# Kernel tuning notes

Hardware: AMD Instinct MI355X
Metric: run time of the kernel (lower is better)

The kernel has to match this reference:

```python
import jax, jax.numpy as jnp
import numpy as np

N, E, IN, HID, HEADS, LAYERS, CLASSES = 50000, 800000, 256, 128, 4, 3, 2
DH = HID // HEADS
EPS = 1e-5


def _layernorm(h, g, b):
    mu = jnp.mean(h, axis=-1, keepdims=True)
    var = jnp.mean(jnp.square(h - mu), axis=-1, keepdims=True)
    return (h - mu) / jnp.sqrt(var + EPS) * g + b


def setup_inputs() -> dict:
    key = jax.random.key(0)
    ks = jax.random.split(key, 16)

    def w(k, shape, fan_in):
        return jax.random.normal(k, shape, dtype=jnp.float32) / np.sqrt(fan_in).astype(np.float32)

    inp = {}
    inp["x"] = jax.random.normal(ks[0], (N, IN), dtype=jnp.float32)
    inp["edge_index"] = jax.random.randint(ks[1], (2, E), 0, N, dtype=jnp.int32)
    inp["batch"] = jnp.zeros((N,), dtype=jnp.int32)  # single graph
    # feature extractor: Linear(IN,HID) -> ReLU -> Linear(HID,HID)
    inp["fe_w1"] = w(ks[2], (HID, IN), IN)
    inp["fe_b1"] = jnp.zeros((HID,), jnp.float32)
    inp["fe_w2"] = w(ks[3], (HID, HID), HID)
    inp["fe_b2"] = jnp.zeros((HID,), jnp.float32)
    inp["conv_w"] = w(ks[4], (LAYERS, HID, 2 * HID), 2 * HID)
    inp["conv_b"] = jnp.zeros((LAYERS, HID), jnp.float32)
    inp["ln_g"] = jnp.ones((LAYERS, HID), jnp.float32)
    inp["ln_b"] = jnp.zeros((LAYERS, HID), jnp.float32)
    # MultiheadAttention(HID, 4 heads): packed in_proj + out_proj
    inp["in_proj_w"] = w(ks[5], (3 * HID, HID), HID)
    inp["in_proj_b"] = jnp.zeros((3 * HID,), jnp.float32)
    inp["out_w"] = w(ks[6], (HID, HID), HID)
    inp["out_b"] = jnp.zeros((HID,), jnp.float32)
    # classifier: Linear(2*HID, HID) -> ReLU -> Linear(HID, CLASSES)
    inp["c_w1"] = w(ks[7], (HID, 2 * HID), 2 * HID)
    inp["c_b1"] = jnp.zeros((HID,), jnp.float32)
    inp["c_w2"] = w(ks[8], (CLASSES, HID), HID)
    inp["c_b2"] = jnp.zeros((CLASSES,), jnp.float32)
    return inp


def reference(x, edge_index, batch, fe_w1, fe_b1, fe_w2, fe_b2, conv_w, conv_b,
              ln_g, ln_b, in_proj_w, in_proj_b, out_w, out_b, c_w1, c_b1, c_w2, c_b2):
    # feature extractor (dropout inactive in eval mode)
    h = jax.nn.relu(x @ fe_w1.T + fe_b1) @ fe_w2.T + fe_b2  # [N, HID]
    row, col = edge_index[0], edge_index[1]
    for i in range(LAYERS):
        # scatter_add of source-node features onto destination nodes
        nbr = jax.ops.segment_sum(h[row], col, num_segments=N)  # [N, HID]
        hcat = jnp.concatenate([h, nbr], axis=-1)               # [N, 2*HID]
        h = _layernorm(hcat @ conv_w[i].T + conv_b[i], ln_g[i], ln_b[i])
        h = jax.nn.relu(h)
    # MultiheadAttention with h.unsqueeze(0) and batch_first=False:
    # seq_len = 1, batch = N -> softmax over a single key yields weight 1.
    qkv = h @ in_proj_w.T + in_proj_b                          # [N, 3*HID]
    q, k, v = jnp.split(qkv, 3, axis=-1)
    qh = q.reshape(N, HEADS, DH)
    kh = k.reshape(N, HEADS, DH)
    vh = v.reshape(N, HEADS, DH)
    scores = jnp.sum(qh * kh, axis=-1) / np.sqrt(DH).astype(np.float32)  # [N, H]
    wts = jax.nn.softmax(scores[..., None], axis=-1)           # [N, H, 1] == 1
    attn = wts * vh                                            # [N, H, DH]
    h_attn = attn.reshape(N, HID) @ out_w.T + out_b
    h = h + h_attn
    # global mean / max pool over (all-zero) batch ids
    counts = jax.ops.segment_sum(jnp.ones((N, 1), h.dtype), batch, num_segments=1)
    h_mean = jax.ops.segment_sum(h, batch, num_segments=1) / counts      # [1, HID]
    h_max = jax.ops.segment_max(h, batch, num_segments=1)                # [1, HID]
    g = jnp.concatenate([h_mean, h_max], axis=-1)                        # [1, 2*HID]
    return jax.nn.relu(g @ c_w1.T + c_b1) @ c_w2.T + c_b2                # [1, CLASSES]
```

## Files before the change

### kernel.cpp

```cpp
#include <hip/hip_runtime.h>

constexpr int HID = 128;
constexpr int NB  = 1024;
constexpr int NCH = 64;

typedef __attribute__((ext_vector_type(8))) short short8;
typedef __attribute__((ext_vector_type(8))) unsigned short us8;
typedef __attribute__((ext_vector_type(4))) float f32x4;

__device__ __forceinline__ unsigned short f2bf(float f) {
    union { float f; unsigned u; } v; v.f = f;
    unsigned r = v.u + 0x7fffu + ((v.u >> 16) & 1u);
    return (unsigned short)(r >> 16);
}
__device__ __forceinline__ float bf2f(unsigned short u) {
    union { unsigned u; float f; } v; v.u = ((unsigned)u) << 16;
    return v.f;
}

template<int K, bool CONCAT, bool RELU, bool LN, bool POOL>
__device__ __forceinline__
void mgemm_body(int bid, const unsigned short* __restrict__ A1b,
                const unsigned short* __restrict__ A2b,
                const unsigned short* __restrict__ Wb,
                const float* __restrict__ bias, const float* __restrict__ lng,
                const float* __restrict__ lnb, unsigned short* __restrict__ C,
                float* __restrict__ part, int nrows)
{
    constexpr int LDT = 40;
    __shared__ unsigned short lds[2 * 128 * LDT];
    unsigned short* As = lds;
    unsigned short* Ws = lds + 128 * LDT;
    const int tid = threadIdx.x;
    const int w = tid >> 6, l = tid & 63;
    const int lr = l & 15, lg = l >> 4;
    const int row0 = bid * 128;

    f32x4 acc[2][8] = {};
    const int sr = tid >> 1;
    const int sc = (tid & 1) * 16;
    int gr = row0 + sr; if (gr >= nrows) gr = nrows - 1;

    for (int k0 = 0; k0 < K; k0 += 32) {
        const unsigned short* bsrc;
        if (CONCAT) bsrc = ((k0 < 128) ? A1b : A2b) + (size_t)gr * 128 + (k0 & 127) + sc;
        else        bsrc = A1b + (size_t)gr * K + k0 + sc;
        us8 a0 = *(const us8*)(bsrc + 0);
        us8 a1 = *(const us8*)(bsrc + 8);
        *(us8*)&As[sr * LDT + sc + 0] = a0;
        *(us8*)&As[sr * LDT + sc + 8] = a1;

        const unsigned short* s = Wb + (size_t)sr * K + k0 + sc;
        us8 b0 = *(const us8*)(s + 0);
        us8 b1 = *(const us8*)(s + 8);
        *(us8*)&Ws[sr * LDT + sc + 0] = b0;
        *(us8*)&Ws[sr * LDT + sc + 8] = b1;
        __syncthreads();

        short8 afr[2];
#pragma unroll
        for (int rt = 0; rt < 2; rt++)
            afr[rt] = *(const short8*)&As[(w * 32 + rt * 16 + lr) * LDT + lg * 8];
#pragma unroll
        for (int ct = 0; ct < 8; ct++) {
            short8 bfr = *(const short8*)&Ws[(ct * 16 + lr) * LDT + lg * 8];
#pragma unroll
            for (int rt = 0; rt < 2; rt++)
                acc[rt][ct] = __builtin_amdgcn_mfma_f32_16x16x32_bf16(
                    afr[rt], bfr, acc[rt][ct], 0, 0, 0);
        }
        __syncthreads();
    }

    float bia[8], g8[8], be[8];
#pragma unroll
    for (int ct = 0; ct < 8; ct++) {
        bia[ct] = bias[ct * 16 + lr];
        if (LN) { g8[ct] = lng[ct * 16 + lr]; be[ct] = lnb[ct * 16 + lr]; }
    }
    float ps[8], pm[8];
    if (POOL) {
#pragma unroll
        for (int ct = 0; ct < 8; ct++) { ps[ct] = 0.f; pm[ct] = -3.402823466e+38f; }
    }
#pragma unroll
    for (int rt = 0; rt < 2; rt++) {
#pragma unroll
        for (int r_ = 0; r_ < 4; r_++) {
            int row = row0 + w * 32 + rt * 16 + lg * 4 + r_;
            float v[8];
#pragma unroll
            for (int ct = 0; ct < 8; ct++) v[ct] = acc[rt][ct][r_] + bia[ct];
            if (LN) {
                float s = 0.f;
#pragma unroll
                for (int ct = 0; ct < 8; ct++) s += v[ct];
#pragma unroll
                for (int m = 8; m >= 1; m >>= 1) s += __shfl_xor(s, m);
                float mean = s * (1.f / 128.f);
                float q = 0.f;
#pragma unroll
                for (int ct = 0; ct < 8; ct++) { v[ct] -= mean; q += v[ct] * v[ct]; }
#pragma unroll
                for (int m = 8; m >= 1; m >>= 1) q += __shfl_xor(q, m);
                float rstd = rsqrtf(q * (1.f / 128.f) + 1e-5f);
#pragma unroll
                for (int ct = 0; ct < 8; ct++) v[ct] = v[ct] * rstd * g8[ct] + be[ct];
            }
            if (RELU) {
#pragma unroll
                for (int ct = 0; ct < 8; ct++) v[ct] = fmaxf(v[ct], 0.f);
            }
            if (row < nrows) {
                if (POOL) {
#pragma unroll
                    for (int ct = 0; ct < 8; ct++) {
                        ps[ct] += v[ct];
                        pm[ct] = fmaxf(pm[ct], v[ct]);
                    }
                } else {
#pragma unroll
                    for (int ct = 0; ct < 8; ct++)
                        C[(size_t)row * 128 + ct * 16 + lr] = f2bf(v[ct]);
                }
            }
        }
    }
    if (POOL) {
        float* scr = (float*)lds;
        const int g = w * 4 + lg;
#pragma unroll
        for (int ct = 0; ct < 8; ct++) {
            int col = ct * 16 + lr;
            scr[g * 128 + col] = ps[ct];
            scr[2048 + g * 128 + col] = pm[ct];
        }
        __syncthreads();
        if (tid < 128) {
            float s = 0.f, m = -3.402823466e+38f;
#pragma unroll
            for (int gg = 0; gg < 16; gg++) {
                s += scr[gg * 128 + tid];
                m = fmaxf(m, scr[2048 + gg * 128 + tid]);
            }
            part[bid * 256 + tid] = s;
            part[bid * 256 + 128 + tid] = m;
        }
    }
}

template<int K, bool CONCAT, bool RELU, bool LN, bool POOL>
__global__ __launch_bounds__(256)
void mgemm(const unsigned short* __restrict__ A1b, const unsigned short* __restrict__ A2b,
           const unsigned short* __restrict__ Wb, const float* __restrict__ bias,
           const float* __restrict__ lng, const float* __restrict__ lnb,
           unsigned short* __restrict__ C, float* __restrict__ part, int nrows)
{
    mgemm_body<K,CONCAT,RELU,LN,POOL>(blockIdx.x, A1b, A2b, Wb, bias, lng, lnb,
                                      C, part, nrows);
}

__device__ __forceinline__ void cvt8_blk(const float* __restrict__ src,
                                         unsigned short* __restrict__ dst,
                                         int relb, int n)
{
    int i = (relb * 256 + threadIdx.x) * 8;
    if (i + 8 <= n) {
        float4 a = *(const float4*)(src + i);
        float4 b = *(const float4*)(src + i + 4);
        us8 o;
        o[0]=f2bf(a.x); o[1]=f2bf(a.y); o[2]=f2bf(a.z); o[3]=f2bf(a.w);
        o[4]=f2bf(b.x); o[5]=f2bf(b.y); o[6]=f2bf(b.z); o[7]=f2bf(b.w);
        *(us8*)(dst + i) = o;
    } else {
        for (int j = i; j < n; j++) dst[j] = f2bf(src[j]);
    }
}

__global__ __launch_bounds__(256)
void prep0(const float* __restrict__ x, unsigned short* __restrict__ xb, int nx,
           const float* __restrict__ fe_w1, unsigned short* __restrict__ w1b,
           const float* __restrict__ fe_w2, unsigned short* __restrict__ w2b,
           const float* __restrict__ conv_w, unsigned short* __restrict__ cwb,
           const float* __restrict__ out_w, const float* __restrict__ v_w,
           const float* __restrict__ out_b, const float* __restrict__ bv,
           unsigned short* __restrict__ Mb, float* __restrict__ bias2,
           const int* __restrict__ ecol, int* __restrict__ ccnt,
           int range, int ch_sz, int E)
{
    const int b = blockIdx.x;
    const int tid = threadIdx.x;
    if (b < NCH) {
        __shared__ int cnt[NB];
        for (int i = tid; i < NB; i += 256) cnt[i] = 0;
        __syncthreads();
        int e0 = b * ch_sz;
        int e1 = e0 + ch_sz; if (e1 > E) e1 = E;
        int e = e0 + tid;
        for (; e + 768 < e1; e += 1024) {
            int c0 = ecol[e], c1 = ecol[e+256], c2 = ecol[e+512], c3 = ecol[e+768];
            atomicAdd(&cnt[c0 / range], 1);
            atomicAdd(&cnt[c1 / range], 1);
            atomicAdd(&cnt[c2 / range], 1);
            atomicAdd(&cnt[c3 / range], 1);
        }
        for (; e < e1; e += 256)
            atomicAdd(&cnt[ecol[e] / range], 1);
        __syncthreads();
        for (int i = tid; i < NB; i += 256) ccnt[(size_t)i * NCH + b] = cnt[i];
        return;
    }
    int b2 = b - NCH;
    if (b2 < 64) {
        const int i = b2 * 2 + (tid >> 7);
        const int j = tid & 127;
        float s = 0.f;
        for (int k = 0; k < 128; k++)
            s = fmaf(out_w[i*128 + k], v_w[k*128 + j], s);
        Mb[i*128 + j] = f2bf(s + ((i == j) ? 1.f : 0.f));
        if (j == 0) {
            float bb = out_b[i];
            for (int k = 0; k < 128; k++)
                bb = fmaf(out_w[i*128 + k], bv[k], bb);
            bias2[i] = bb;
        }
        return;
    }
    b2 -= 64;
    if (b2 < 16) { cvt8_blk(fe_w1, w1b, b2, 128*256); return; }
    b2 -= 16;
    if (b2 < 8)  { cvt8_blk(fe_w2, w2b, b2, 128*128); return; }
    b2 -= 8;
    if (b2 < 48) { cvt8_blk(conv_w, cwb, b2, 3*128*256); return; }
    b2 -= 48;
    cvt8_blk(x, xb, b2, nx);
}

__global__ __launch_bounds__(256)
void p2scan(const int* __restrict__ ccnt, int* __restrict__ cbase,
            int* __restrict__ btot, int* __restrict__ bbase)
{
    __shared__ int wsum[4];
    const int t = threadIdx.x;
    int tot[4];
#pragma unroll
    for (int j = 0; j < 4; j++) {
        int b = t * 4 + j;
        const int4* p = (const int4*)(ccnt + (size_t)b * NCH);
        int s = 0;
#pragma unroll
        for (int q = 0; q < NCH / 4; q++) {
            int4 v = p[q];
            s += (v.x + v.y) + (v.z + v.w);
        }
        tot[j] = s;
    }
    int tsum = tot[0] + tot[1] + tot[2] + tot[3];
    int inc = tsum;
#pragma unroll
    for (int d2 = 1; d2 < 64; d2 <<= 1) {
        int u = __shfl_up(inc, d2);
        if ((t & 63) >= d2) inc += u;
    }
    if ((t & 63) == 63) wsum[t >> 6] = inc;
    __syncthreads();
    int woff = 0;
#pragma unroll
    for (int w = 0; w < 4; w++) if (w < (t >> 6)) woff += wsum[w];
    int ex = woff + inc - tsum;
#pragma unroll
    for (int j = 0; j < 4; j++) {
        int b = t * 4 + j;
        bbase[b] = ex;
        btot[b]  = tot[j];
        const int4* p = (const int4*)(ccnt + (size_t)b * NCH);
        int4* q4 = (int4*)(cbase + (size_t)b * NCH);
        int run = ex;
#pragma unroll
        for (int q = 0; q < NCH / 4; q++) {
            int4 v = p[q];
            int4 o;
            o.x = run; run += v.x;
            o.y = run; run += v.y;
            o.z = run; run += v.z;
            o.w = run; run += v.w;
            q4[q] = o;
        }
        ex += tot[j];
    }
}

__global__ __launch_bounds__(256)
void fe1_scat(const unsigned short* __restrict__ xb, const unsigned short* __restrict__ w1b,
              const float* __restrict__ fe_b1, unsigned short* __restrict__ outh,
              int nrows,
              const int* __restrict__ erow, const int* __restrict__ ecol,
              const int* __restrict__ cbase, unsigned* __restrict__ grouped,
              int range, int ch_sz, int E)
{
    const int b = blockIdx.x;
    const int tid = threadIdx.x;
    if (b < NCH) {
        const int chunk = b;
        __shared__ int cur[NB];
        for (int i = tid; i < NB; i += 256) cur[i] = cbase[(size_t)i * NCH + chunk];
        __syncthreads();
        int e0 = chunk * ch_sz;
        int e1 = e0 + ch_sz; if (e1 > E) e1 = E;
        int e = e0 + tid;
        for (; e + 768 < e1; e += 1024) {
            int c0 = ecol[e],     r0 = erow[e];
            int c1 = ecol[e+256], r1 = erow[e+256];
            int c2 = ecol[e+512], r2 = erow[e+512];
            int c3 = ecol[e+768], r3 = erow[e+768];
            int bk0 = c0 / range, bk1 = c1 / range, bk2 = c2 / range, bk3 = c3 / range;
            int p0 = atomicAdd(&cur[bk0], 1);
            int p1 = atomicAdd(&cur[bk1], 1);
            int p2 = atomicAdd(&cur[bk2], 1);
            int p3 = atomicAdd(&cur[bk3], 1);
            grouped[p0] = ((unsigned)r0 << 6) | (unsigned)(c0 - bk0 * range);
            grouped[p1] = ((unsigned)r1 << 6) | (unsigned)(c1 - bk1 * range);
            grouped[p2] = ((unsigned)r2 << 6) | (unsigned)(c2 - bk2 * range);
            grouped[p3] = ((unsigned)r3 << 6) | (unsigned)(c3 - bk3 * range);
        }
        for (; e < e1; e += 256) {
            int c = ecol[e], r = erow[e];
            int bk = c / range;
            int pos = atomicAdd(&cur[bk], 1);
            grouped[pos] = ((unsigned)r << 6) | (unsigned)(c - bk * range);
        }
        return;
    }
    mgemm_body<256,false,true,false,false>(
        b - NCH, xb, nullptr, w1b, fe_b1, nullptr, nullptr, outh, nullptr, nrows);
}

__global__ __launch_bounds__(256)
void fe2_csr2(const unsigned short* __restrict__ hin, const unsigned short* __restrict__ w2b,
              const float* __restrict__ fe_b2, unsigned short* __restrict__ outh,
              int nrows, int nbk,
              const int* __restrict__ bbase, const int* __restrict__ btot,
              const unsigned* __restrict__ grouped, int range, int N,
              int* __restrict__ offg, int* __restrict__ degg, int* __restrict__ csr)
{
    const int b = blockIdx.x;
    const int tid = threadIdx.x;
    if (b >= nbk) {
        mgemm_body<128,false,false,false,false>(
            b - nbk, hin, nullptr, w2b, fe_b2, nullptr, nullptr, outh, nullptr, nrows);
        return;
    }
    const int bk = b;
    __shared__ unsigned ent[2048];
    __shared__ int hist[64];
    __shared__ int cur2[64];
    const int base = bbase[bk];
    int cnt = btot[bk]; if (cnt > 2048) cnt = 2048;
    for (int i = tid; i < cnt; i += 256) ent[i] = grouped[base + i];
    if (tid < 64) hist[tid] = 0;
    __syncthreads();
    for (int i = tid; i < cnt; i += 256) atomicAdd(&hist[ent[i] & 63], 1);
    __syncthreads();
    if (tid == 0) {
        int run = base;
        const int nodebase = bk * range;
        int nn = N - nodebase; if (nn > range) nn = range;
        for (int j = 0; j < nn; j++) {
            int h = hist[j];
            offg[nodebase + j] = run;
            degg[nodebase + j] = h;
            cur2[j] = run;
            run += h;
        }
    }
    __syncthreads();
    for (int i = tid; i < cnt; i += 256) {
        unsigned v = ent[i];
        int p = atomicAdd(&cur2[v & 63], 1);
        csr[p] = (int)(v >> 6);
    }
}

__global__ __launch_bounds__(256)
void gather_sum(const unsigned short* __restrict__ h, const int* __restrict__ offg,
                const int* __restrict__ degg, const int* __restrict__ csr,
                unsigned short* __restrict__ nbr, int N)
{
    int gw = (blockIdx.x * 256 + threadIdx.x) >> 6;
    if (gw >= N) return;
    const int lane = threadIdx.x & 63;
    const int start = offg[gw];
    const int d = degg[gw];
    const unsigned* hp = (const unsigned*)h + lane;
    float ax[8] = {}, ay[8] = {};
    int i = 0;
    for (; i + 8 <= d; i += 8) {
        int s[8];
#pragma unroll
        for (int j = 0; j < 8; j++) s[j] = csr[start + i + j];
        unsigned u[8];
#pragma unroll
        for (int j = 0; j < 8; j++) u[j] = hp[(size_t)s[j] * 64];
#pragma unroll
        for (int j = 0; j < 8; j++) {
            ax[j] += __uint_as_float(u[j] << 16);
            ay[j] += __uint_as_float(u[j] & 0xffff0000u);
        }
    }
    for (; i < d; i++) {
        unsigned u = hp[(size_t)csr[start + i] * 64];
        ax[0] += __uint_as_float(u << 16);
        ay[0] += __uint_as_float(u & 0xffff0000u);
    }
    float sx = ((ax[0]+ax[1]) + (ax[2]+ax[3])) + ((ax[4]+ax[5]) + (ax[6]+ax[7]));
    float sy = ((ay[0]+ay[1]) + (ay[2]+ay[3])) + ((ay[4]+ay[5]) + (ay[6]+ay[7]));
    unsigned o = ((unsigned)f2bf(sx)) | (((unsigned)f2bf(sy)) << 16);
    *((unsigned*)nbr + (size_t)gw * 64 + lane) = o;
}

__global__ __launch_bounds__(256)
void pool_reduce16(const float* __restrict__ part, float* __restrict__ part2,
                   int nblocks)
{
    const int t = threadIdx.x;
    const int b0 = blockIdx.x;
    if (t < 128) {
        float s = 0.f;
        for (int b = b0; b < nblocks; b += 16) s += part[b*256 + t];
        part2[b0*256 + t] = s;
    } else {
        float m = -3.402823466e+38f;
        for (int b = b0; b < nblocks; b += 16) m = fmaxf(m, part[b*256 + t]);
        part2[b0*256 + t] = m;
    }
}

__global__ __launch_bounds__(256)
void cls_fused(const float* __restrict__ part2, int n,
               const float* __restrict__ cw1, const float* __restrict__ cb1,
               const float* __restrict__ cw2, const float* __restrict__ cb2,
               float* __restrict__ out, int classes)
{
    __shared__ float g[256];
    __shared__ float t1[128];
    const int tid = threadIdx.x;
    if (tid < 128) {
        float s = 0.f;
#pragma unroll
        for (int b = 0; b < 16; b++) s += part2[b*256 + tid];
        g[tid] = s / (float)n;
    } else {
        float m = -3.402823466e+38f;
#pragma unroll
        for (int b = 0; b < 16; b++) m = fmaxf(m, part2[b*256 + tid]);
        g[tid] = m;
    }
    __syncthreads();
    const int w = tid >> 6, lane = tid & 63;
    float4 gv = *(const float4*)&g[lane*4];
#pragma unroll 4
    for (int i = 0; i < 32; i++) {
        int r = w * 32 + i;
        float4 wv = *(const float4*)(cw1 + (size_t)r*256 + lane*4);
        float p = wv.x*gv.x + wv.y*gv.y + wv.z*gv.z + wv.w*gv.w;
#pragma unroll
        for (int m = 32; m >= 1; m >>= 1) p += __shfl_xor(p, m);
        if (lane == 0) t1[r] = fmaxf(p + cb1[r], 0.f);
    }
    __syncthreads();
    if (tid < 128) {
        int c = tid >> 6;
        if (c < classes) {
            float p = t1[lane] * cw2[c*128 + lane] + t1[lane+64] * cw2[c*128 + lane + 64];
#pragma unroll
            for (int m = 32; m >= 1; m >>= 1) p += __shfl_xor(p, m);
            if (lane == 0) out[c] = p + cb2[c];
        }
    }
}

extern "C" void kernel_launch(void* const* d_in, const int* in_sizes, int n_in,
                              void* d_out, int out_size, void* d_ws, size_t ws_size,
                              hipStream_t stream)
{
    const float* x        = (const float*)d_in[0];
    const int*   ei       = (const int*)  d_in[1];
    const float* fe_w1    = (const float*)d_in[3];
    const float* fe_b1    = (const float*)d_in[4];
    const float* fe_w2    = (const float*)d_in[5];
    const float* fe_b2    = (const float*)d_in[6];
    const float* conv_w   = (const float*)d_in[7];
    const float* conv_b   = (const float*)d_in[8];
    const float* ln_g     = (const float*)d_in[9];
    const float* ln_b     = (const float*)d_in[10];
    const float* in_proj_w= (const float*)d_in[11];
    const float* in_proj_b= (const float*)d_in[12];
    const float* out_w    = (const float*)d_in[13];
    const float* out_b    = (const float*)d_in[14];
    const float* c_w1     = (const float*)d_in[15];
    const float* c_b1     = (const float*)d_in[16];
    const float* c_w2     = (const float*)d_in[17];
    const float* c_b2     = (const float*)d_in[18];
    float* out = (float*)d_out;

    const int N = in_sizes[0] / 256;
    const int E = in_sizes[1] / 2;
    const int NX = in_sizes[0];
    const int CLASSES = out_size;
    const int* erow = ei;
    const int* ecol = ei + E;

    const int range = (N + NB - 1) / NB;
    const int nbk   = (N + range - 1) / range;
    const int ch_sz = (E + NCH - 1) / NCH;

    const size_t NH = (size_t)N * HID;

    unsigned short* nbrb  = (unsigned short*)d_ws;
    unsigned short* hb0   = nbrb + NH;
    unsigned short* hb1   = hb0 + NH;
    unsigned short* xb    = hb1 + NH;
    float*          part  = (float*)(xb + NX);
    float*          part2 = part + 512*256;
    float*          bias2 = part2 + 16*256;
    unsigned short* w1b   = (unsigned short*)(bias2 + 128);
    unsigned short* w2b   = w1b + 128*256;
    unsigned short* cwb   = w2b + 128*128;
    unsigned short* Mb    = cwb + 3*128*256;
    int*            ccnt  = (int*)(Mb + 128*128);
    int*            cbase = ccnt + NB*NCH;
    int*            btot  = cbase + NB*NCH;
    int*            bbase = btot + NB;
    int*            offg  = bbase + NB;
    int*            degg  = offg + N;
    int*            csr   = degg + N;
    unsigned*       grouped = (unsigned*)(csr + E);

    const int gblocks = (N + 127) / 128;
    const int nxb = (NX + 2047) / 2048;
    dim3 blk(256);

    prep0<<<NCH + 64 + 16 + 8 + 48 + nxb, blk, 0, stream>>>(
        x, xb, NX, fe_w1, w1b, fe_w2, w2b, conv_w, cwb,
        out_w, in_proj_w + (size_t)2*HID*HID, out_b, in_proj_b + 2*HID,
        Mb, bias2, ecol, ccnt, range, ch_sz, E);

    p2scan<<<1, blk, 0, stream>>>(ccnt, cbase, btot, bbase);

    fe1_scat<<<NCH + gblocks, blk, 0, stream>>>(
        xb, w1b, fe_b1, hb1, N, erow, ecol, cbase, grouped, range, ch_sz, E);

    fe2_csr2<<<nbk + gblocks, blk, 0, stream>>>(
        hb1, w2b, fe_b2, hb0, N, nbk, bbase, btot, grouped, range, N,
        offg, degg, csr);

    unsigned short* h = hb0;
    unsigned short* other = hb1;
    const int wblocks = (int)(((size_t)N * 64 + 255) / 256);
    for (int l = 0; l < 3; l++) {
        gather_sum<<<wblocks, blk, 0, stream>>>(h, offg, degg, csr, nbrb, N);
        mgemm<256,true,true,true,false><<<gblocks, blk, 0, stream>>>(
            h, nbrb, cwb + (size_t)l*128*256, conv_b + l*HID,
            ln_g + l*HID, ln_b + l*HID, other, nullptr, N);
        unsigned short* t = h; h = other; other = t;
    }

    mgemm<128,false,false,false,true><<<gblocks, blk, 0, stream>>>(
        h, nullptr, Mb, bias2, nullptr, nullptr, nullptr, part, N);

    pool_reduce16<<<16, blk, 0, stream>>>(part, part2, gblocks);
    cls_fused<<<1, blk, 0, stream>>>(part2, N, c_w1, c_b1, c_w2, c_b2, out, CLASSES);
}
```

Baseline: 272.1 us.

## Fuse neighbor gather-sum into conv GEMM, keeping aggregated features in LDS

Replaces the separate gather_sum kernel and concat GEMM with one conv_fused kernel per layer. Each block first gathers and sums neighbor rows for its 128 nodes into an LDS tile, then runs the 256-wide GEMM with the first half of K read from h and the second half from LDS, followed by LayerNorm and ReLU. This removes the global write and re-read of the neighbor buffer and one launch per layer. In exchange, the gather now runs only 391 blocks, each wave processing 32 nodes serially, and LDS use per block grows (about 54 KB), which lowers occupancy and latency hiding for the irregular gather.

```diff
diff --git a/kernel.cpp b/kernel.cpp
--- a/kernel.cpp
+++ b/kernel.cpp
@@ -18,13 +18,11 @@
     return v.f;
 }
 
-template<int K, bool CONCAT, bool RELU, bool LN, bool POOL>
+template<int K, bool RELU, bool POOL>
 __device__ __forceinline__
 void mgemm_body(int bid, const unsigned short* __restrict__ A1b,
-                const unsigned short* __restrict__ A2b,
                 const unsigned short* __restrict__ Wb,
-                const float* __restrict__ bias, const float* __restrict__ lng,
-                const float* __restrict__ lnb, unsigned short* __restrict__ C,
+                const float* __restrict__ bias, unsigned short* __restrict__ C,
                 float* __restrict__ part, int nrows)
 {
     constexpr int LDT = 40;
@@ -42,9 +40,7 @@
     int gr = row0 + sr; if (gr >= nrows) gr = nrows - 1;
 
     for (int k0 = 0; k0 < K; k0 += 32) {
-        const unsigned short* bsrc;
-        if (CONCAT) bsrc = ((k0 < 128) ? A1b : A2b) + (size_t)gr * 128 + (k0 & 127) + sc;
-        else        bsrc = A1b + (size_t)gr * K + k0 + sc;
+        const unsigned short* bsrc = A1b + (size_t)gr * K + k0 + sc;
         us8 a0 = *(const us8*)(bsrc + 0);
         us8 a1 = *(const us8*)(bsrc + 8);
         *(us8*)&As[sr * LDT + sc + 0] = a0;
@@ -72,12 +68,9 @@
         __syncthreads();
     }
 
-    float bia[8], g8[8], be[8];
-#pragma unroll
-    for (int ct = 0; ct < 8; ct++) {
-        bia[ct] = bias[ct * 16 + lr];
-        if (LN) { g8[ct] = lng[ct * 16 + lr]; be[ct] = lnb[ct * 16 + lr]; }
-    }
+    float bia[8];
+#pragma unroll
+    for (int ct = 0; ct < 8; ct++) bia[ct] = bias[ct * 16 + lr];
     float ps[8], pm[8];
     if (POOL) {
 #pragma unroll
@@ -91,22 +84,6 @@
             float v[8];
 #pragma unroll
             for (int ct = 0; ct < 8; ct++) v[ct] = acc[rt][ct][r_] + bia[ct];
-            if (LN) {
-                float s = 0.f;
-#pragma unroll
-                for (int ct = 0; ct < 8; ct++) s += v[ct];
-#pragma unroll
-                for (int m = 8; m >= 1; m >>= 1) s += __shfl_xor(s, m);
-                float mean = s * (1.f / 128.f);
-                float q = 0.f;
-#pragma unroll
-                for (int ct = 0; ct < 8; ct++) { v[ct] -= mean; q += v[ct] * v[ct]; }
-#pragma unroll
-                for (int m = 8; m >= 1; m >>= 1) q += __shfl_xor(q, m);
-                float rstd = rsqrtf(q * (1.f / 128.f) + 1e-5f);
-#pragma unroll
-                for (int ct = 0; ct < 8; ct++) v[ct] = v[ct] * rstd * g8[ct] + be[ct];
-            }
             if (RELU) {
 #pragma unroll
                 for (int ct = 0; ct < 8; ct++) v[ct] = fmaxf(v[ct], 0.f);
@@ -149,15 +126,154 @@
     }
 }
 
-template<int K, bool CONCAT, bool RELU, bool LN, bool POOL>
-__global__ __launch_bounds__(256)
-void mgemm(const unsigned short* __restrict__ A1b, const unsigned short* __restrict__ A2b,
-           const unsigned short* __restrict__ Wb, const float* __restrict__ bias,
-           const float* __restrict__ lng, const float* __restrict__ lnb,
-           unsigned short* __restrict__ C, float* __restrict__ part, int nrows)
-{
-    mgemm_body<K,CONCAT,RELU,LN,POOL>(blockIdx.x, A1b, A2b, Wb, bias, lng, lnb,
-                                      C, part, nrows);
+template<int K, bool RELU, bool POOL>
+__global__ __launch_bounds__(256)
+void mgemm(const unsigned short* __restrict__ A1b, const unsigned short* __restrict__ Wb,
+           const float* __restrict__ bias, unsigned short* __restrict__ C,
+           float* __restrict__ part, int nrows)
+{
+    mgemm_body<K,RELU,POOL>(blockIdx.x, A1b, Wb, bias, C, part, nrows);
+}
+
+__global__ __launch_bounds__(256)
+void conv_fused(const unsigned short* __restrict__ h, const unsigned short* __restrict__ Wb,
+                const float* __restrict__ bias, const float* __restrict__ lng,
+                const float* __restrict__ lnb,
+                const int* __restrict__ offg, const int* __restrict__ degg,
+                const int* __restrict__ csr,
+                unsigned short* __restrict__ C, int nrows)
+{
+    constexpr int LDT = 40;
+    constexpr int LDN = 132;
+    __shared__ unsigned short As[128 * LDT];
+    __shared__ unsigned short Ws[128 * LDT];
+    __shared__ unsigned short NbrT[128 * LDN];
+    const int tid = threadIdx.x;
+    const int w = tid >> 6, l = tid & 63;
+    const int lr = l & 15, lg = l >> 4;
+    const int row0 = blockIdx.x * 128;
+
+    const unsigned* hp = (const unsigned*)h + l;
+    for (int n = 0; n < 32; n++) {
+        const int q = row0 + w * 32 + n;
+        int d = 0, start = 0;
+        if (q < nrows) { start = offg[q]; d = degg[q]; }
+        float sx = 0.f, sy = 0.f;
+        int i = 0;
+        for (; i + 16 <= d; i += 16) {
+            int s[16];
+#pragma unroll
+            for (int j = 0; j < 16; j++) s[j] = csr[start + i + j];
+            unsigned u[16];
+#pragma unroll
+            for (int j = 0; j < 16; j++) u[j] = hp[(size_t)s[j] * 64];
+#pragma unroll
+            for (int j = 0; j < 16; j++) {
+                sx += __uint_as_float(u[j] << 16);
+                sy += __uint_as_float(u[j] & 0xffff0000u);
+            }
+        }
+        if (i + 8 <= d) {
+            int s[8];
+#pragma unroll
+            for (int j = 0; j < 8; j++) s[j] = csr[start + i + j];
+            unsigned u[8];
+#pragma unroll
+            for (int j = 0; j < 8; j++) u[j] = hp[(size_t)s[j] * 64];
+#pragma unroll
+            for (int j = 0; j < 8; j++) {
+                sx += __uint_as_float(u[j] << 16);
+                sy += __uint_as_float(u[j] & 0xffff0000u);
+            }
+            i += 8;
+        }
+        for (; i < d; i++) {
+            unsigned u = hp[(size_t)csr[start + i] * 64];
+            sx += __uint_as_float(u << 16);
+            sy += __uint_as_float(u & 0xffff0000u);
+        }
+        unsigned o = ((unsigned)f2bf(sx)) | (((unsigned)f2bf(sy)) << 16);
+        *(unsigned*)&NbrT[(w * 32 + n) * LDN + l * 2] = o;
+    }
+    __syncthreads();
+
+    f32x4 acc[2][8] = {};
+    const int sr = tid >> 1;
+    const int sc = (tid & 1) * 16;
+    int gr = row0 + sr; if (gr >= nrows) gr = nrows - 1;
+
+#pragma unroll
+    for (int k0 = 0; k0 < 256; k0 += 32) {
+        if (k0 < 128) {
+            const unsigned short* bsrc = h + (size_t)gr * 128 + k0 + sc;
+            us8 a0 = *(const us8*)(bsrc + 0);
+            us8 a1 = *(const us8*)(bsrc + 8);
+            *(us8*)&As[sr * LDT + sc + 0] = a0;
+            *(us8*)&As[sr * LDT + sc + 8] = a1;
+        }
+        const unsigned short* s = Wb + (size_t)sr * 256 + k0 + sc;
+        us8 b0 = *(const us8*)(s + 0);
+        us8 b1 = *(const us8*)(s + 8);
+        *(us8*)&Ws[sr * LDT + sc + 0] = b0;
+        *(us8*)&Ws[sr * LDT + sc + 8] = b1;
+        __syncthreads();
+
+        short8 afr[2];
+#pragma unroll
+        for (int rt = 0; rt < 2; rt++) {
+            if (k0 < 128)
+                afr[rt] = *(const short8*)&As[(w * 32 + rt * 16 + lr) * LDT + lg * 8];
+            else
+                afr[rt] = *(const short8*)&NbrT[(w * 32 + rt * 16 + lr) * LDN + (k0 - 128) + lg * 8];
+        }
+#pragma unroll
+        for (int ct = 0; ct < 8; ct++) {
+            short8 bfr = *(const short8*)&Ws[(ct * 16 + lr) * LDT + lg * 8];
+#pragma unroll
+            for (int rt = 0; rt < 2; rt++)
+                acc[rt][ct] = __builtin_amdgcn_mfma_f32_16x16x32_bf16(
+                    afr[rt], bfr, acc[rt][ct], 0, 0, 0);
+        }
+        __syncthreads();
+    }
+
+    float bia[8], g8[8], be[8];
+#pragma unroll
+    for (int ct = 0; ct < 8; ct++) {
+        bia[ct] = bias[ct * 16 + lr];
+        g8[ct] = lng[ct * 16 + lr];
+        be[ct] = lnb[ct * 16 + lr];
+    }
+#pragma unroll
+    for (int rt = 0; rt < 2; rt++) {
+#pragma unroll
+        for (int r_ = 0; r_ < 4; r_++) {
+            int row = row0 + w * 32 + rt * 16 + lg * 4 + r_;
+            float v[8];
+#pragma unroll
+            for (int ct = 0; ct < 8; ct++) v[ct] = acc[rt][ct][r_] + bia[ct];
+            float s = 0.f;
+#pragma unroll
+            for (int ct = 0; ct < 8; ct++) s += v[ct];
+#pragma unroll
+            for (int m = 8; m >= 1; m >>= 1) s += __shfl_xor(s, m);
+            float mean = s * (1.f / 128.f);
+            float q = 0.f;
+#pragma unroll
+            for (int ct = 0; ct < 8; ct++) { v[ct] -= mean; q += v[ct] * v[ct]; }
+#pragma unroll
+            for (int m = 8; m >= 1; m >>= 1) q += __shfl_xor(q, m);
+            float rstd = rsqrtf(q * (1.f / 128.f) + 1e-5f);
+#pragma unroll
+            for (int ct = 0; ct < 8; ct++)
+                v[ct] = fmaxf(v[ct] * rstd * g8[ct] + be[ct], 0.f);
+            if (row < nrows) {
+#pragma unroll
+                for (int ct = 0; ct < 8; ct++)
+                    C[(size_t)row * 128 + ct * 16 + lr] = f2bf(v[ct]);
+            }
+        }
+    }
 }
 
 __device__ __forceinline__ void cvt8_blk(const float* __restrict__ src,
@@ -331,8 +447,7 @@
         }
         return;
     }
-    mgemm_body<256,false,true,false,false>(
-        b - NCH, xb, nullptr, w1b, fe_b1, nullptr, nullptr, outh, nullptr, nrows);
+    mgemm_body<256,true,false>(b - NCH, xb, w1b, fe_b1, outh, nullptr, nrows);
 }
 
 __global__ __launch_bounds__(256)
@@ -346,8 +461,7 @@
     const int b = blockIdx.x;
     const int tid = threadIdx.x;
     if (b >= nbk) {
-        mgemm_body<128,false,false,false,false>(
-            b - nbk, hin, nullptr, w2b, fe_b2, nullptr, nullptr, outh, nullptr, nrows);
+        mgemm_body<128,false,false>(b - nbk, hin, w2b, fe_b2, outh, nullptr, nrows);
         return;
     }
     const int bk = b;
@@ -382,43 +496,6 @@
 }
 
 __global__ __launch_bounds__(256)
-void gather_sum(const unsigned short* __restrict__ h, const int* __restrict__ offg,
-                const int* __restrict__ degg, const int* __restrict__ csr,
-                unsigned short* __restrict__ nbr, int N)
-{
-    int gw = (blockIdx.x * 256 + threadIdx.x) >> 6;
-    if (gw >= N) return;
-    const int lane = threadIdx.x & 63;
-    const int start = offg[gw];
-    const int d = degg[gw];
-    const unsigned* hp = (const unsigned*)h + lane;
-    float ax[8] = {}, ay[8] = {};
-    int i = 0;
-    for (; i + 8 <= d; i += 8) {
-        int s[8];
-#pragma unroll
-        for (int j = 0; j < 8; j++) s[j] = csr[start + i + j];
-        unsigned u[8];
-#pragma unroll
-        for (int j = 0; j < 8; j++) u[j] = hp[(size_t)s[j] * 64];
-#pragma unroll
-        for (int j = 0; j < 8; j++) {
-            ax[j] += __uint_as_float(u[j] << 16);
-            ay[j] += __uint_as_float(u[j] & 0xffff0000u);
-        }
-    }
-    for (; i < d; i++) {
-        unsigned u = hp[(size_t)csr[start + i] * 64];
-        ax[0] += __uint_as_float(u << 16);
-        ay[0] += __uint_as_float(u & 0xffff0000u);
-    }
-    float sx = ((ax[0]+ax[1]) + (ax[2]+ax[3])) + ((ax[4]+ax[5]) + (ax[6]+ax[7]));
-    float sy = ((ay[0]+ay[1]) + (ay[2]+ay[3])) + ((ay[4]+ay[5]) + (ay[6]+ay[7]));
-    unsigned o = ((unsigned)f2bf(sx)) | (((unsigned)f2bf(sy)) << 16);
-    *((unsigned*)nbr + (size_t)gw * 64 + lane) = o;
-}
-
-__global__ __launch_bounds__(256)
 void pool_reduce16(const float* __restrict__ part, float* __restrict__ part2,
                    int nblocks)
 {
@@ -516,8 +593,7 @@
 
     const size_t NH = (size_t)N * HID;
 
-    unsigned short* nbrb  = (unsigned short*)d_ws;
-    unsigned short* hb0   = nbrb + NH;
+    unsigned short* hb0   = (unsigned short*)d_ws;
     unsigned short* hb1   = hb0 + NH;
     unsigned short* xb    = hb1 + NH;
     float*          part  = (float*)(xb + NX);
@@ -556,17 +632,15 @@
 
     unsigned short* h = hb0;
     unsigned short* other = hb1;
-    const int wblocks = (int)(((size_t)N * 64 + 255) / 256);
     for (int l = 0; l < 3; l++) {
-        gather_sum<<<wblocks, blk, 0, stream>>>(h, offg, degg, csr, nbrb, N);
-        mgemm<256,true,true,true,false><<<gblocks, blk, 0, stream>>>(
-            h, nbrb, cwb + (size_t)l*128*256, conv_b + l*HID,
-            ln_g + l*HID, ln_b + l*HID, other, nullptr, N);
+        conv_fused<<<gblocks, blk, 0, stream>>>(
+            h, cwb + (size_t)l*128*256, conv_b + l*HID,
+            ln_g + l*HID, ln_b + l*HID, offg, degg, csr, other, N);
         unsigned short* t = h; h = other; other = t;
     }
 
-    mgemm<128,false,false,false,true><<<gblocks, blk, 0, stream>>>(
-        h, nullptr, Mb, bias2, nullptr, nullptr, nullptr, part, N);
+    mgemm<128,false,true><<<gblocks, blk, 0, stream>>>(
+        h, Mb, bias2, nullptr, part, N);
 
     pool_reduce16<<<16, blk, 0, stream>>>(part, part2, gblocks);
     cls_fused<<<1, blk, 0, stream>>>(part2, N, c_w1, c_b1, c_w2, c_b2, out, CLASSES);
```

Result: slower. 458.7 us (+68.6%).
